# Kernel optimization log

Measured on AMD Instinct MI355X. Metric: run time of the kernel, lower is better.

## Reference

```python
import jax, jax.numpy as jnp
import numpy as np
import math

N_HEAD = 16
D_MODEL = 1024
BATCH = 2
SEQ = 2048


def setup_inputs() -> dict:
    key = jax.random.key(0)
    ks = jax.random.split(key, 12)
    s = 1.0 / math.sqrt(D_MODEL)
    inp = {
        "Q": jax.random.normal(ks[0], (BATCH, SEQ, D_MODEL), jnp.float32),
        "K": jax.random.normal(ks[1], (BATCH, SEQ, D_MODEL), jnp.float32),
        "V": jax.random.normal(ks[2], (BATCH, SEQ, D_MODEL), jnp.float32),
        # causal mask, broadcastable against scores [n_head, B, S, S]
        "mask": jnp.tril(jnp.ones((SEQ, SEQ), jnp.int32))[None, None, :, :],
        "w_q": jax.random.normal(ks[3], (D_MODEL, D_MODEL), jnp.float32) * s,
        "b_q": jax.random.normal(ks[4], (D_MODEL,), jnp.float32) * s,
        "w_k": jax.random.normal(ks[5], (D_MODEL, D_MODEL), jnp.float32) * s,
        "b_k": jax.random.normal(ks[6], (D_MODEL,), jnp.float32) * s,
        "w_v": jax.random.normal(ks[7], (D_MODEL, D_MODEL), jnp.float32) * s,
        "b_v": jax.random.normal(ks[8], (D_MODEL,), jnp.float32) * s,
        "w_o": jax.random.normal(ks[9], (D_MODEL, D_MODEL), jnp.float32) * s,
        "b_o": jax.random.normal(ks[10], (D_MODEL,), jnp.float32) * s,
    }
    return inp


def _linear(x, w, b):
    # torch nn.Linear convention: w is [out, in]
    return jnp.einsum("bsi,oi->bso", x, w) + b


def reference(Q, K, V, mask, w_q, b_q, w_k, b_k, w_v, b_v, w_o, b_o):
    B, S, D = Q.shape
    d_k = D // N_HEAD
    # Faithful to the original's view(B, n_head, -1, d_k).transpose(0, 1):
    # reshape flattened (seq*d_model) into (n_head, S, d_k), then swap to [h, B, S, d_k]
    q = jnp.swapaxes(_linear(Q, w_q, b_q).reshape(B, N_HEAD, S, d_k), 0, 1)
    k = jnp.swapaxes(_linear(K, w_k, b_k).reshape(B, N_HEAD, S, d_k), 0, 1)
    v = jnp.swapaxes(_linear(V, w_v, b_v).reshape(B, N_HEAD, S, d_k), 0, 1)
    scores = jnp.einsum("hbqd,hbkd->hbqk", q, k) / jnp.sqrt(jnp.float32(d_k))
    scores = jnp.where(mask == 0, jnp.float32(-1e9), scores)
    p = jax.nn.softmax(scores, axis=-1)  # dropout off (eval mode)
    v_att = jnp.einsum("hbqk,hbkd->hbqd", p, v)
    # permute(1, 2, 0, 3).view(B, -1, D)
    v_att = jnp.transpose(v_att, (1, 2, 0, 3)).reshape(B, S, D)
    v_att = jnp.einsum("bsi,oi->bso", v_att, w_o) + b_o
    k_lin = jnp.transpose(k, (1, 2, 0, 3)).reshape(B, S, D)
    return (k_lin, v_att)
```

## Files before the change

### kernel.cpp

```cpp
#include <hip/hip_runtime.h>
#include <stdint.h>

#define NHEAD 16
#define DM    1024
#define BB    2
#define SS    2048
#define DKH   64
#define MR    4096

typedef float f32x4 __attribute__((ext_vector_type(4)));
typedef __bf16 bf16x8 __attribute__((ext_vector_type(8)));
typedef unsigned short u16;
typedef unsigned int   u32;
typedef unsigned short u16x8 __attribute__((ext_vector_type(8)));
typedef unsigned short u16x4 __attribute__((ext_vector_type(4)));
typedef unsigned int   u32x4 __attribute__((ext_vector_type(4)));

static __device__ __forceinline__ f32x4 mfma16(bf16x8 a, bf16x8 b, f32x4 c) {
  return __builtin_amdgcn_mfma_f32_16x16x32_bf16(a, b, c, 0, 0, 0);
}
static __device__ __forceinline__ u16 f2bf(float x) {
  u32 u = __float_as_uint(x);
  return (u16)((u + 0x7fffu + ((u >> 16) & 1u)) >> 16);
}
static __device__ __forceinline__ float bf2f(u16 h) { return __uint_as_float(((u32)h) << 16); }
static __device__ __forceinline__ void split2(float x, u16 &h, u16 &l) {
  h = f2bf(x);
  l = f2bf(x - bf2f(h));
}
static __device__ __forceinline__ void splitT(float x, u16 &h, u16 &l) {
  const u32 xb = __float_as_uint(x);
  h = (u16)(xb >> 16);
  const float r = x - __uint_as_float(xb & 0xffff0000u);
  l = (u16)(__float_as_uint(r) >> 16);
}
static __device__ __forceinline__ void async16(const void* g, const void* l) {
  __builtin_amdgcn_global_load_lds(
      (const __attribute__((address_space(1))) u32*)g,
      (__attribute__((address_space(3))) u32*)l, 16, 0, 0);
}
static __device__ __forceinline__ u32 lds_off(const void* p) {
  return (u32)(uintptr_t)(__attribute__((address_space(3))) const void*)p;
}
static __device__ __forceinline__ u16x4 tr16(u32 addr, int imm) {
  u16x4 d;
  asm volatile("ds_read_b64_tr_b16 %0, %1 offset:%2" : "=v"(d) : "v"(addr), "i"(imm));
  return d;
}

struct SplitArgs {
  const float* in[7];
  u16* hi[7];
  u16* lo[7];
};
__global__ __launch_bounds__(256) void split_all(SplitArgs a) {
  const long t = (long)blockIdx.x * 256 + threadIdx.x;
  int r; long u;
  if (t < 3L * 1048576L) {
    r = (int)(t / 1048576L); u = t - (long)r * 1048576L;
  } else {
    long v = t - 3L * 1048576L;
    int i = (int)(v / 262144L);
    r = 3 + i; u = v - (long)i * 262144L;
  }
  const float4 x = ((const float4*)a.in[r])[u];
  ushort4 hv, lv;
  split2(x.x, hv.x, lv.x);
  split2(x.y, hv.y, lv.y);
  split2(x.z, hv.z, lv.z);
  split2(x.w, hv.w, lv.w);
  ((ushort4*)a.hi[r])[u] = hv;
  ((ushort4*)a.lo[r])[u] = lv;
}

static __device__ __forceinline__ void gemm_core(
    const u16* __restrict__ Ah, const u16* __restrict__ Al,
    const u16* __restrict__ Bh, const u16* __restrict__ Bl,
    u16* lds, f32x4 (&acc)[4][4])
{
  const int tid = threadIdx.x, lane = tid & 63, wave = tid >> 6;
  const int wr = wave >> 1, wc = wave & 1;
  const int bm = blockIdx.x, bn = blockIdx.y;
  u16* lAh = lds;
  u16* lAl = lds + 4096;
  u16* lBh = lds + 8192;
  u16* lBl = lds + 12288;

#pragma unroll
  for (int i = 0; i < 4; ++i)
#pragma unroll
    for (int j = 0; j < 4; ++j) acc[i][j] = f32x4{0.f, 0.f, 0.f, 0.f};

  for (int kt = 0; kt < 1024 / 32; ++kt) {
    __syncthreads();
#pragma unroll
    for (int inst = 0; inst < 2; ++inst) {
      const int c = inst * 256 + tid;
      const int row = c >> 2, cc = c & 3;
      const int scol = ((cc ^ ((row >> 1) & 3)) << 3);
      const int lb = (inst * 256 + wave * 64) * 8;
      const int ga = (bm * 128 + row) * 1024 + kt * 32 + scol;
      const int gb = (bn * 128 + row) * 1024 + kt * 32 + scol;
      async16(Ah + ga, lAh + lb);
      async16(Al + ga, lAl + lb);
      async16(Bh + gb, lBh + lb);
      async16(Bl + gb, lBl + lb);
    }
    asm volatile("s_waitcnt vmcnt(0)" ::: "memory");
    __syncthreads();

    const int c = lane >> 4;
    bf16x8 ah[4], al[4];
#pragma unroll
    for (int i = 0; i < 4; ++i) {
      const int row = wr * 64 + i * 16 + (lane & 15);
      const int off = row * 32 + ((c ^ ((row >> 1) & 3)) << 3);
      ah[i] = *(const bf16x8*)(lAh + off);
      al[i] = *(const bf16x8*)(lAl + off);
    }
#pragma unroll
    for (int j = 0; j < 4; ++j) {
      const int row = wc * 64 + j * 16 + (lane & 15);
      const int off = row * 32 + ((c ^ ((row >> 1) & 3)) << 3);
      bf16x8 bh = *(const bf16x8*)(lBh + off);
      bf16x8 bl = *(const bf16x8*)(lBl + off);
#pragma unroll
      for (int i = 0; i < 4; ++i) {
        acc[i][j] = mfma16(ah[i], bh, acc[i][j]);
        acc[i][j] = mfma16(ah[i], bl, acc[i][j]);
        acc[i][j] = mfma16(al[i], bh, acc[i][j]);
      }
    }
  }
}

struct QkvArgs {
  const u16* Ah[3]; const u16* Al[3];
  const u16* Bh[3]; const u16* Bl[3];
  const float* bias[3];
  u16* Oh[3]; u16* Ol[3];
  float* klin;
};
__global__ __launch_bounds__(256, 4) void gemm_qkv(QkvArgs a) {
  __shared__ __align__(16) u16 lds[16384];
  const int p = blockIdx.z;
  f32x4 acc[4][4];
  gemm_core(a.Ah[p], a.Al[p], a.Bh[p], a.Bl[p], lds, acc);

  const int tid = threadIdx.x, lane = tid & 63, wave = tid >> 6;
  const int wr = wave >> 1, wc = wave & 1;
  const int bm = blockIdx.x, bn = blockIdx.y;
  const float* bias = a.bias[p];
  u16* Oh = a.Oh[p];
  u16* Ol = a.Ol[p];
#pragma unroll
  for (int j = 0; j < 4; ++j) {
    const int n = bn * 128 + wc * 64 + j * 16 + (lane & 15);
    const float bv = bias[n];
#pragma unroll
    for (int i = 0; i < 4; ++i) {
#pragma unroll
      for (int r = 0; r < 4; ++r) {
        const int m = bm * 128 + wr * 64 + i * 16 + ((lane >> 4) << 2) + r;
        const float v = acc[i][j][r] + bv;
        u16 hh, ll; splitT(v, hh, ll);
        Oh[m * 1024 + n] = hh;
        Ol[m * 1024 + n] = ll;
        if (p == 1) {
          const int b = m >> 11, rr = m & 2047;
          const int hidx = rr >> 7;
          const int s2 = ((rr & 127) << 4) + (n >> 6);
          const int dk = n & 63;
          a.klin[b * (SS * DM) + s2 * DM + hidx * 64 + dk] = v;
        }
      }
    }
  }
}

__global__ __launch_bounds__(256, 4) void gemm_out(
    const u16* __restrict__ Ah, const u16* __restrict__ Al,
    const u16* __restrict__ Bh, const u16* __restrict__ Bl,
    const float* __restrict__ bias, float* __restrict__ out)
{
  __shared__ __align__(16) u16 lds[16384];
  f32x4 acc[4][4];
  gemm_core(Ah, Al, Bh, Bl, lds, acc);
  const int tid = threadIdx.x, lane = tid & 63, wave = tid >> 6;
  const int wr = wave >> 1, wc = wave & 1;
  const int bm = blockIdx.x, bn = blockIdx.y;
#pragma unroll
  for (int j = 0; j < 4; ++j) {
    const int n = bn * 128 + wc * 64 + j * 16 + (lane & 15);
    const float bv = bias[n];
#pragma unroll
    for (int i = 0; i < 4; ++i) {
#pragma unroll
      for (int r = 0; r < 4; ++r) {
        const int m = bm * 128 + wr * 64 + i * 16 + ((lane >> 4) << 2) + r;
        out[m * 1024 + n] = acc[i][j][r] + bv;
      }
    }
  }
}

#define PSTR 68
__global__ __launch_bounds__(256, 2) void flash(
    const u16* __restrict__ qh, const u16* __restrict__ ql,
    const u16* __restrict__ kh, const u16* __restrict__ kl,
    const u16* __restrict__ vh, const u16* __restrict__ vl,
    u16* __restrict__ aoh, u16* __restrict__ aol)
{
  __shared__ __align__(16) u16 lKh[64 * 64];
  __shared__ __align__(16) u16 lKl[64 * 64];
  __shared__ __align__(16) u16 lV[2][64 * 64];
  __shared__ __align__(16) u32 lP[4][16 * PSTR];

  const int tid = threadIdx.x, lane = tid & 63, wave = tid >> 6;
  const int qt = 31 - blockIdx.y, bh = blockIdx.x;
  const int b = bh >> 4, h = bh & 15;
  const int base = b * (SS * DM) + h * (SS * DKH);

  bf16x8 aqh[2], aql[2];
  {
    const int qrow = qt * 64 + wave * 16 + (lane & 15);
#pragma unroll
    for (int s = 0; s < 2; ++s) {
      const int off = base + qrow * 64 + s * 32 + ((lane >> 4) << 3);
      aqh[s] = *(const bf16x8*)(qh + off);
      aql[s] = *(const bf16x8*)(ql + off);
    }
  }

  const u32 trbase = lds_off(&lV[0][0]) + (u32)lane * 8u;

  f32x4 o[4];
#pragma unroll
  for (int cf = 0; cf < 4; ++cf) o[cf] = f32x4{0.f, 0.f, 0.f, 0.f};
  float lrun[4] = {0.f, 0.f, 0.f, 0.f};
  const float SC = 0.125f * 1.44269504089f;
  const int qr0 = (lane >> 4) << 2;

  for (int kt = 0; kt <= qt; ++kt) {
    __syncthreads();
#pragma unroll
    for (int inst = 0; inst < 2; ++inst) {
      const int c = inst * 256 + tid;
      const int row = c >> 3, cc = c & 7;
      const int scol = ((cc ^ (row & 7)) << 3);
      const int g = base + (kt * 64 + row) * 64 + scol;
      const int lb = (inst * 256 + wave * 64) * 8;
      async16(kh + g, lKh + lb);
      async16(kl + g, lKl + lb);
    }
#pragma unroll
    for (int inst = 0; inst < 2; ++inst) {
      const int kc = (inst * 8 + (lane >> 3)) * 4 + ((lane & 7) >> 1);
      const int d  = wave * 16 + (lane & 1) * 8;
      const int g  = base + (kt * 64 + kc) * 64 + d;
      const int lb = (wave * 16 + inst * 8) * 64;
      async16(vh + g, &lV[0][lb]);
      async16(vl + g, &lV[1][lb]);
    }
    asm volatile("s_waitcnt vmcnt(0)" ::: "memory");
    __syncthreads();

    f32x4 sf[4];
#pragma unroll
    for (int cf = 0; cf < 4; ++cf) sf[cf] = f32x4{0.f, 0.f, 0.f, 0.f};
    __builtin_amdgcn_s_setprio(1);
#pragma unroll
    for (int s = 0; s < 2; ++s) {
#pragma unroll
      for (int cf = 0; cf < 4; ++cf) {
        const int row = cf * 16 + (lane & 15);
        const int c = s * 4 + (lane >> 4);
        const int off = row * 64 + ((c ^ (row & 7)) << 3);
        bf16x8 kbh = *(const bf16x8*)(lKh + off);
        bf16x8 kbl = *(const bf16x8*)(lKl + off);
        sf[cf] = mfma16(aqh[s], kbh, sf[cf]);
        sf[cf] = mfma16(aqh[s], kbl, sf[cf]);
        sf[cf] = mfma16(aql[s], kbh, sf[cf]);
      }
    }
    __builtin_amdgcn_s_setprio(0);

    u32 pk[4][4];
#pragma unroll
    for (int cf = 0; cf < 4; ++cf)
#pragma unroll
      for (int r = 0; r < 4; ++r) {
        float zz = sf[cf][r] * SC;
        if (kt == qt) {
          const int kcol = cf * 16 + (lane & 15);
          if (kcol > wave * 16 + qr0 + r) zz = -1e30f;
        }
        zz = fminf(zz, 60.0f);
        const float pv = exp2f(zz);
        lrun[r] += pv;
        const u32 xb = __float_as_uint(pv);
        const float rr = pv - __uint_as_float(xb & 0xffff0000u);
        pk[cf][r] = __builtin_amdgcn_perm(__float_as_uint(rr), xb, 0x07060302u);
      }

#pragma unroll
    for (int cf = 0; cf < 4; ++cf)
#pragma unroll
      for (int r = 0; r < 4; ++r)
        lP[wave][(qr0 + r) * PSTR + cf * 16 + (lane & 15)] = pk[cf][r];

#pragma unroll
    for (int ks = 0; ks < 2; ++ks) {
      const int pa = (lane & 15) * PSTR + ks * 32 + ((lane >> 4) << 2);
      const uint4 w0 = *(const uint4*)(&lP[wave][pa]);
      const uint4 w1 = *(const uint4*)(&lP[wave][pa + 16]);
      u32x4 hq, lq;
      hq[0] = __builtin_amdgcn_perm(w0.y, w0.x, 0x05040100u);
      hq[1] = __builtin_amdgcn_perm(w0.w, w0.z, 0x05040100u);
      hq[2] = __builtin_amdgcn_perm(w1.y, w1.x, 0x05040100u);
      hq[3] = __builtin_amdgcn_perm(w1.w, w1.z, 0x05040100u);
      lq[0] = __builtin_amdgcn_perm(w0.y, w0.x, 0x07060302u);
      lq[1] = __builtin_amdgcn_perm(w0.w, w0.z, 0x07060302u);
      lq[2] = __builtin_amdgcn_perm(w1.y, w1.x, 0x07060302u);
      lq[3] = __builtin_amdgcn_perm(w1.w, w1.z, 0x07060302u);
      const bf16x8 pah = __builtin_bit_cast(bf16x8, hq);
      const bf16x8 pal = __builtin_bit_cast(bf16x8, lq);

      u16x4 th[4][2], tl[4][2];
#pragma unroll
      for (int cf = 0; cf < 4; ++cf)
#pragma unroll
        for (int r = 0; r < 2; ++r) {
          th[cf][r] = tr16(trbase, (cf * 16 + ks * 8 + r * 4) * 128);
          tl[cf][r] = tr16(trbase, 8192 + (cf * 16 + ks * 8 + r * 4) * 128);
        }
      asm volatile("s_waitcnt lgkmcnt(0)" ::: "memory");
      __builtin_amdgcn_sched_barrier(0);

      __builtin_amdgcn_s_setprio(1);
#pragma unroll
      for (int cf = 0; cf < 4; ++cf) {
        const u16x8 vh_ = __builtin_shufflevector(th[cf][0], th[cf][1], 0, 1, 2, 3, 4, 5, 6, 7);
        const u16x8 vl_ = __builtin_shufflevector(tl[cf][0], tl[cf][1], 0, 1, 2, 3, 4, 5, 6, 7);
        const bf16x8 vbh = __builtin_bit_cast(bf16x8, vh_);
        const bf16x8 vbl = __builtin_bit_cast(bf16x8, vl_);
        o[cf] = mfma16(pah, vbh, o[cf]);
        o[cf] = mfma16(pah, vbl, o[cf]);
        o[cf] = mfma16(pal, vbh, o[cf]);
      }
      __builtin_amdgcn_s_setprio(0);
    }
  }

#pragma unroll
  for (int mm = 1; mm < 16; mm <<= 1)
#pragma unroll
    for (int r = 0; r < 4; ++r) lrun[r] += __shfl_xor(lrun[r], mm, 64);
  float inv[4];
#pragma unroll
  for (int r = 0; r < 4; ++r) inv[r] = 1.0f / lrun[r];
  const int mbase = b * SS + qt * 64 + wave * 16;
#pragma unroll
  for (int cf = 0; cf < 4; ++cf)
#pragma unroll
    for (int r = 0; r < 4; ++r) {
      const int mrow = mbase + qr0 + r;
      const int col = h * 64 + cf * 16 + (lane & 15);
      const float v = o[cf][r] * inv[r];
      u16 hh, ll; splitT(v, hh, ll);
      aoh[mrow * DM + col] = hh;
      aol[mrow * DM + col] = ll;
    }
}

extern "C" void kernel_launch(void* const* d_in, const int* in_sizes, int n_in,
                              void* d_out, int out_size, void* d_ws, size_t ws_size,
                              hipStream_t stream) {
  (void)in_sizes; (void)n_in; (void)out_size; (void)ws_size;
  const float* Qin = (const float*)d_in[0];
  const float* Kin = (const float*)d_in[1];
  const float* Vin = (const float*)d_in[2];
  const float* wq = (const float*)d_in[4];
  const float* bq = (const float*)d_in[5];
  const float* wk = (const float*)d_in[6];
  const float* bk = (const float*)d_in[7];
  const float* wv = (const float*)d_in[8];
  const float* bv = (const float*)d_in[9];
  const float* wo = (const float*)d_in[10];
  const float* bo = (const float*)d_in[11];
  float* out_klin = (float*)d_out;
  float* out_vatt = out_klin + (size_t)BB * SS * DM;

  u16* ws16 = (u16*)d_ws;
  const size_t AE = 4194304;
  const size_t WE = 1048576;
  u16 *Xh[3], *Xl[3];
  for (int p = 0; p < 3; ++p) { Xh[p] = ws16 + (size_t)p * 2 * AE; Xl[p] = Xh[p] + AE; }
  u16* wbase = ws16 + 6 * AE;
  u16 *Wh[4], *Wl[4];
  for (int i = 0; i < 4; ++i) { Wh[i] = wbase + (size_t)i * 2 * WE; Wl[i] = Wh[i] + WE; }
  u16* qkv = wbase + 8 * WE;
  u16* q_hi = qkv + 0 * AE; u16* q_lo = qkv + 1 * AE;
  u16* k_hi = qkv + 2 * AE; u16* k_lo = qkv + 3 * AE;
  u16* v_hi = qkv + 4 * AE; u16* v_lo = qkv + 5 * AE;
  u16* attnHi = ws16;
  u16* attnLo = ws16 + AE;

  SplitArgs sa;
  const float* sin_[7] = {Qin, Kin, Vin, wq, wk, wv, wo};
  u16* shi[7] = {Xh[0], Xh[1], Xh[2], Wh[0], Wh[1], Wh[2], Wh[3]};
  u16* slo[7] = {Xl[0], Xl[1], Xl[2], Wl[0], Wl[1], Wl[2], Wl[3]};
  for (int i = 0; i < 7; ++i) { sa.in[i] = sin_[i]; sa.hi[i] = shi[i]; sa.lo[i] = slo[i]; }
  hipLaunchKernelGGL(split_all, dim3(16384), dim3(256), 0, stream, sa);

  QkvArgs qa;
  const float* biases[3] = {bq, bk, bv};
  u16* oh[3] = {q_hi, k_hi, v_hi};
  u16* ol[3] = {q_lo, k_lo, v_lo};
  for (int p = 0; p < 3; ++p) {
    qa.Ah[p] = Xh[p]; qa.Al[p] = Xl[p];
    qa.Bh[p] = Wh[p]; qa.Bl[p] = Wl[p];
    qa.bias[p] = biases[p];
    qa.Oh[p] = oh[p]; qa.Ol[p] = ol[p];
  }
  qa.klin = out_klin;
  hipLaunchKernelGGL(gemm_qkv, dim3(32, 8, 3), dim3(256), 0, stream, qa);

  hipLaunchKernelGGL(flash, dim3(32, 32), dim3(256), 0, stream,
                     q_hi, q_lo, k_hi, k_lo, v_hi, v_lo, attnHi, attnLo);

  hipLaunchKernelGGL(gemm_out, dim3(32, 8), dim3(256), 0, stream,
                     attnHi, attnLo, Wh[3], Wl[3], bo, out_vatt);
}
```

Measured before the change: 343.3 us.

## Double-buffer LDS tiles in output projection GEMM to overlap loads with MFMA

```diff
diff --git a/kernel.cpp b/kernel.cpp
--- a/kernel.cpp
+++ b/kernel.cpp
@@ -73,6 +73,52 @@
   ((ushort4*)a.lo[r])[u] = lv;
 }
 
+static __device__ __forceinline__ void stage32(
+    const u16* __restrict__ Ah, const u16* __restrict__ Al,
+    const u16* __restrict__ Bh, const u16* __restrict__ Bl,
+    u16* buf, int bm, int bn, int kt, int tid, int wave)
+{
+#pragma unroll
+  for (int inst = 0; inst < 2; ++inst) {
+    const int c = inst * 256 + tid;
+    const int row = c >> 2, cc = c & 3;
+    const int scol = ((cc ^ ((row >> 1) & 3)) << 3);
+    const int lb = (inst * 256 + wave * 64) * 8;
+    const int ga = (bm * 128 + row) * 1024 + kt * 32 + scol;
+    const int gb = (bn * 128 + row) * 1024 + kt * 32 + scol;
+    async16(Ah + ga, buf + lb);
+    async16(Al + ga, buf + 4096 + lb);
+    async16(Bh + gb, buf + 8192 + lb);
+    async16(Bl + gb, buf + 12288 + lb);
+  }
+}
+static __device__ __forceinline__ void comp32(
+    const u16* buf, int lane, int wr, int wc, f32x4 (&acc)[4][4])
+{
+  const int c = lane >> 4;
+  bf16x8 ah[4], al[4];
+#pragma unroll
+  for (int i = 0; i < 4; ++i) {
+    const int row = wr * 64 + i * 16 + (lane & 15);
+    const int off = row * 32 + ((c ^ ((row >> 1) & 3)) << 3);
+    ah[i] = *(const bf16x8*)(buf + off);
+    al[i] = *(const bf16x8*)(buf + 4096 + off);
+  }
+#pragma unroll
+  for (int j = 0; j < 4; ++j) {
+    const int row = wc * 64 + j * 16 + (lane & 15);
+    const int off = row * 32 + ((c ^ ((row >> 1) & 3)) << 3);
+    bf16x8 bh = *(const bf16x8*)(buf + 8192 + off);
+    bf16x8 bl = *(const bf16x8*)(buf + 12288 + off);
+#pragma unroll
+    for (int i = 0; i < 4; ++i) {
+      acc[i][j] = mfma16(ah[i], bh, acc[i][j]);
+      acc[i][j] = mfma16(ah[i], bl, acc[i][j]);
+      acc[i][j] = mfma16(al[i], bh, acc[i][j]);
+    }
+  }
+}
+
 static __device__ __forceinline__ void gemm_core(
     const u16* __restrict__ Ah, const u16* __restrict__ Al,
     const u16* __restrict__ Bh, const u16* __restrict__ Bl,
@@ -81,11 +127,6 @@
   const int tid = threadIdx.x, lane = tid & 63, wave = tid >> 6;
   const int wr = wave >> 1, wc = wave & 1;
   const int bm = blockIdx.x, bn = blockIdx.y;
-  u16* lAh = lds;
-  u16* lAl = lds + 4096;
-  u16* lBh = lds + 8192;
-  u16* lBl = lds + 12288;
-
 #pragma unroll
   for (int i = 0; i < 4; ++i)
 #pragma unroll
@@ -93,43 +134,41 @@
 
   for (int kt = 0; kt < 1024 / 32; ++kt) {
     __syncthreads();
-#pragma unroll
-    for (int inst = 0; inst < 2; ++inst) {
-      const int c = inst * 256 + tid;
-      const int row = c >> 2, cc = c & 3;
-      const int scol = ((cc ^ ((row >> 1) & 3)) << 3);
-      const int lb = (inst * 256 + wave * 64) * 8;
-      const int ga = (bm * 128 + row) * 1024 + kt * 32 + scol;
-      const int gb = (bn * 128 + row) * 1024 + kt * 32 + scol;
-      async16(Ah + ga, lAh + lb);
-      async16(Al + ga, lAl + lb);
-      async16(Bh + gb, lBh + lb);
-      async16(Bl + gb, lBl + lb);
-    }
+    stage32(Ah, Al, Bh, Bl, lds, bm, bn, kt, tid, wave);
     asm volatile("s_waitcnt vmcnt(0)" ::: "memory");
     __syncthreads();
-
-    const int c = lane >> 4;
-    bf16x8 ah[4], al[4];
-#pragma unroll
-    for (int i = 0; i < 4; ++i) {
-      const int row = wr * 64 + i * 16 + (lane & 15);
-      const int off = row * 32 + ((c ^ ((row >> 1) & 3)) << 3);
-      ah[i] = *(const bf16x8*)(lAh + off);
-      al[i] = *(const bf16x8*)(lAl + off);
-    }
-#pragma unroll
-    for (int j = 0; j < 4; ++j) {
-      const int row = wc * 64 + j * 16 + (lane & 15);
-      const int off = row * 32 + ((c ^ ((row >> 1) & 3)) << 3);
-      bf16x8 bh = *(const bf16x8*)(lBh + off);
-      bf16x8 bl = *(const bf16x8*)(lBl + off);
-#pragma unroll
-      for (int i = 0; i < 4; ++i) {
-        acc[i][j] = mfma16(ah[i], bh, acc[i][j]);
-        acc[i][j] = mfma16(ah[i], bl, acc[i][j]);
-        acc[i][j] = mfma16(al[i], bh, acc[i][j]);
-      }
+    comp32(lds, lane, wr, wc, acc);
+  }
+}
+
+static __device__ __forceinline__ void gemm_core_pipe(
+    const u16* __restrict__ Ah, const u16* __restrict__ Al,
+    const u16* __restrict__ Bh, const u16* __restrict__ Bl,
+    u16* lds, f32x4 (&acc)[4][4])
+{
+  const int tid = threadIdx.x, lane = tid & 63, wave = tid >> 6;
+  const int wr = wave >> 1, wc = wave & 1;
+  const int bm = blockIdx.x, bn = blockIdx.y;
+#pragma unroll
+  for (int i = 0; i < 4; ++i)
+#pragma unroll
+    for (int j = 0; j < 4; ++j) acc[i][j] = f32x4{0.f, 0.f, 0.f, 0.f};
+
+  stage32(Ah, Al, Bh, Bl, lds, bm, bn, 0, tid, wave);
+  asm volatile("s_waitcnt vmcnt(0)" ::: "memory");
+  __builtin_amdgcn_sched_barrier(0);
+  __builtin_amdgcn_s_barrier();
+
+#pragma unroll 2
+  for (int kt = 0; kt < 32; ++kt) {
+    u16* cur = lds + ((kt & 1) << 14);
+    u16* nxt = lds + (((kt + 1) & 1) << 14);
+    if (kt < 31) stage32(Ah, Al, Bh, Bl, nxt, bm, bn, kt + 1, tid, wave);
+    comp32(cur, lane, wr, wc, acc);
+    if (kt < 31) {
+      asm volatile("s_waitcnt vmcnt(0)" ::: "memory");
+      __builtin_amdgcn_sched_barrier(0);
+      __builtin_amdgcn_s_barrier();
     }
   }
 }
@@ -178,14 +217,14 @@
   }
 }
 
-__global__ __launch_bounds__(256, 4) void gemm_out(
+__global__ __launch_bounds__(256, 2) void gemm_out(
     const u16* __restrict__ Ah, const u16* __restrict__ Al,
     const u16* __restrict__ Bh, const u16* __restrict__ Bl,
     const float* __restrict__ bias, float* __restrict__ out)
 {
-  __shared__ __align__(16) u16 lds[16384];
+  __shared__ __align__(16) u16 lds[32768];
   f32x4 acc[4][4];
-  gemm_core(Ah, Al, Bh, Bl, lds, acc);
+  gemm_core_pipe(Ah, Al, Bh, Bl, lds, acc);
   const int tid = threadIdx.x, lane = tid & 63, wave = tid >> 6;
   const int wr = wave >> 1, wc = wave & 1;
   const int bm = blockIdx.x, bn = blockIdx.y;
```

Result: faster. 335.8 us (-2.2%).
